# Kernel tuning notes

Measured on AMD Instinct MI355X. Metric: run time of the kernel, lower is better.

Reference implementation:

```python
import jax, jax.numpy as jnp
import numpy as np

# pywt db2 decomposition filters (mode='symmetric', pywt defaults)
DEC_LO = np.array([-0.12940952255092145, 0.22414386804185735,
                   0.836516303737469, 0.48296291314469025], dtype=np.float32)
DEC_HI = np.array([-0.48296291314469025, 0.836516303737469,
                   -0.22414386804185735, -0.12940952255092145], dtype=np.float32)


def _dwt_axis(x, filt, axis):
    """Single-level 1D DWT along `axis`, symmetric padding, matching pywt.

    Equivalent to: symmetric-pad by F-1 each side, full convolution with
    `filt` (true convolution => filter flipped), take indices 1,3,5,...
    Implemented as pad (F-2, F-1) + strided correlation with reversed filter.
    """
    F = filt.shape[0]
    x = jnp.moveaxis(x, axis, -1)
    N = x.shape[-1]
    out_len = (N + F - 1) // 2
    pad = [(0, 0)] * (x.ndim - 1) + [(F - 2, F - 1)]
    xp = jnp.pad(x, pad, mode='symmetric')
    filt_rev = filt[::-1]
    # sum of 4 strided slices (F=4) -- fully vectorized, no big intermediates
    out = filt_rev[0] * xp[..., 0:2 * out_len:2]
    for k in range(1, F):
        out = out + filt_rev[k] * xp[..., k:k + 2 * out_len:2]
    return jnp.moveaxis(out, -1, axis)


def setup_inputs() -> dict:
    key = jax.random.key(0)
    x = jax.random.normal(key, (16, 3, 1024, 1024), dtype=jnp.float32)
    return {"x": x}


def reference(x):
    lo = jnp.asarray(DEC_LO)
    hi = jnp.asarray(DEC_HI)
    # pywt.dwt2 -> cA = 'aa' (approx rows, approx cols),
    #              cH = 'da' (detail along axis -2, approx along axis -1)
    lo_rows = _dwt_axis(x, lo, -2)
    hi_rows = _dwt_axis(x, hi, -2)
    cA = _dwt_axis(lo_rows, lo, -1)
    cH = _dwt_axis(hi_rows, lo, -1)
    return (cA, cH)
```

## Files before the change

### kernel.cpp

```cpp
#include <hip/hip_runtime.h>


#define N 1024
#define NOUT 513
#define TI 8
#define STRIPS ((NOUT + TI - 1) / TI)

__device__ __forceinline__ int refl(int p) {
    int r = p - 2;
    r = (r < 0) ? (-1 - r) : r;
    r = (r > N - 1) ? (2 * N - 1 - r) : r;
    return r;
}

__global__ __launch_bounds__(256, 8) void dwt2_strip(const float* __restrict__ x,
                                                     float* __restrict__ out) {
    const float l0 =  0.48296291314469025f;
    const float l1 =  0.836516303737469f;
    const float l2 =  0.22414386804185735f;
    const float l3 = -0.12940952255092145f;
    const float h0 = -0.12940952255092145f;
    const float h1 = -0.22414386804185735f;
    const float h2 =  0.836516303737469f;
    const float h3 = -0.48296291314469025f;

    __shared__ float sLo[2][N];
    __shared__ float sHi[2][N];

    const int strip = blockIdx.x;
    const int img   = blockIdx.y;
    const int i0 = strip * TI;
    const int t  = threadIdx.x;
    const int c  = 4 * t;

    const float* xim = x + (size_t)img * N * N;
    const size_t plane = (size_t)NOUT * NOUT;
    float* cA = out + (size_t)img * plane;
    float* cH = out + ((size_t)48 + img) * plane;

    const int nrows = (NOUT - i0 < TI) ? (NOUT - i0) : TI;

    float4 r0 = *reinterpret_cast<const float4*>(xim + (size_t)refl(2 * i0)     * N + c);
    float4 r1 = *reinterpret_cast<const float4*>(xim + (size_t)refl(2 * i0 + 1) * N + c);
    float4 n0 = *reinterpret_cast<const float4*>(xim + (size_t)refl(2 * i0 + 2) * N + c);
    float4 n1 = *reinterpret_cast<const float4*>(xim + (size_t)refl(2 * i0 + 3) * N + c);

    for (int ii = 0; ii < nrows; ++ii) {
        const int i = i0 + ii;
        const int buf = ii & 1;

        float4 lo, hi;
        lo.x = l0 * r0.x + l1 * r1.x + l2 * n0.x + l3 * n1.x;
        lo.y = l0 * r0.y + l1 * r1.y + l2 * n0.y + l3 * n1.y;
        lo.z = l0 * r0.z + l1 * r1.z + l2 * n0.z + l3 * n1.z;
        lo.w = l0 * r0.w + l1 * r1.w + l2 * n0.w + l3 * n1.w;
        hi.x = h0 * r0.x + h1 * r1.x + h2 * n0.x + h3 * n1.x;
        hi.y = h0 * r0.y + h1 * r1.y + h2 * n0.y + h3 * n1.y;
        hi.z = h0 * r0.z + h1 * r1.z + h2 * n0.z + h3 * n1.z;
        hi.w = h0 * r0.w + h1 * r1.w + h2 * n0.w + h3 * n1.w;
        *reinterpret_cast<float4*>(&sLo[buf][c]) = lo;
        *reinterpret_cast<float4*>(&sHi[buf][c]) = hi;
        r0 = n0;
        r1 = n1;

        __syncthreads();

        if (ii + 1 < nrows) {
            const int ip = i + 1;
            n0 = *reinterpret_cast<const float4*>(xim + (size_t)refl(2 * ip + 2) * N + c);
            n1 = *reinterpret_cast<const float4*>(xim + (size_t)refl(2 * ip + 3) * N + c);
        }

        const float* __restrict__ Lrow = sLo[buf];
        const float* __restrict__ Hrow = sHi[buf];
        for (int j = t; j < NOUT; j += 256) {
            float a0, a1, a2, a3, b0, b1, b2, b3;
            if (j >= 1 && j <= NOUT - 2) {
                const int cc = 2 * j - 2;
                a0 = Lrow[cc]; a1 = Lrow[cc + 1]; a2 = Lrow[cc + 2]; a3 = Lrow[cc + 3];
                b0 = Hrow[cc]; b1 = Hrow[cc + 1]; b2 = Hrow[cc + 2]; b3 = Hrow[cc + 3];
            } else {
                const int c0 = refl(2 * j), c1 = refl(2 * j + 1);
                const int c2 = refl(2 * j + 2), c3 = refl(2 * j + 3);
                a0 = Lrow[c0]; a1 = Lrow[c1]; a2 = Lrow[c2]; a3 = Lrow[c3];
                b0 = Hrow[c0]; b1 = Hrow[c1]; b2 = Hrow[c2]; b3 = Hrow[c3];
            }
            cA[(size_t)i * NOUT + j] = l0 * a0 + l1 * a1 + l2 * a2 + l3 * a3;
            cH[(size_t)i * NOUT + j] = l0 * b0 + l1 * b1 + l2 * b2 + l3 * b3;
        }
    }
}

extern "C" void kernel_launch(void* const* d_in, const int* in_sizes, int n_in,
                              void* d_out, int out_size, void* d_ws, size_t ws_size,
                              hipStream_t stream) {
    (void)in_sizes; (void)n_in; (void)d_ws; (void)ws_size; (void)out_size;
    const float* x = (const float*)d_in[0];
    float* out = (float*)d_out;
    dim3 grid(STRIPS, 48);
    dim3 block(256);
    dwt2_strip<<<grid, block, 0, stream>>>(x, out);
}
```

Before: 312.7 us.

## Replace shared-memory horizontal pass with wavefront shuffles and register-resident rows

Drops the LDS staging buffers and per-row __syncthreads. Each thread now owns two column pairs and does the horizontal filter with __shfl_up across lanes. Wavefront boundary lanes reload and recompute their neighbours' vertical outputs. This removes block-wide barriers and LDS traffic, at the cost of extra redundant global loads at wave edges, float2 instead of float4 loads, and an odd-column store pattern. It also adds register prefetch of the next rows and lowers the launch-bounds occupancy hint.

```diff
diff --git a/kernel.cpp b/kernel.cpp
--- a/kernel.cpp
+++ b/kernel.cpp
@@ -13,8 +13,16 @@
     return r;
 }
 
-__global__ __launch_bounds__(256, 8) void dwt2_strip(const float* __restrict__ x,
-                                                     float* __restrict__ out) {
+__device__ __forceinline__ float2 vfilt(float f0, float f1, float f2, float f3,
+                                        float2 a, float2 b, float2 c, float2 d) {
+    float2 r;
+    r.x = f0 * a.x + f1 * b.x + f2 * c.x + f3 * d.x;
+    r.y = f0 * a.y + f1 * b.y + f2 * c.y + f3 * d.y;
+    return r;
+}
+
+__global__ __launch_bounds__(256, 4) void dwt2_reg(const float* __restrict__ x,
+                                                   float* __restrict__ out) {
     const float l0 =  0.48296291314469025f;
     const float l1 =  0.836516303737469f;
     const float l2 =  0.22414386804185735f;
@@ -24,71 +32,94 @@
     const float h2 =  0.836516303737469f;
     const float h3 = -0.48296291314469025f;
 
-    __shared__ float sLo[2][N];
-    __shared__ float sHi[2][N];
-
     const int strip = blockIdx.x;
     const int img   = blockIdx.y;
     const int i0 = strip * TI;
     const int t  = threadIdx.x;
-    const int c  = 4 * t;
+    const int lane = t & 63;
 
-    const float* xim = x + (size_t)img * N * N;
+    const float* __restrict__ xim = x + (size_t)img * N * N;
     const size_t plane = (size_t)NOUT * NOUT;
-    float* cA = out + (size_t)img * plane;
-    float* cH = out + ((size_t)48 + img) * plane;
+    float* __restrict__ cA = out + (size_t)img * plane;
+    float* __restrict__ cH = out + ((size_t)48 + img) * plane;
 
-    const int nrows = (NOUT - i0 < TI) ? (NOUT - i0) : TI;
+    int nrows = NOUT - i0; if (nrows > TI) nrows = TI;
 
-    float4 r0 = *reinterpret_cast<const float4*>(xim + (size_t)refl(2 * i0)     * N + c);
-    float4 r1 = *reinterpret_cast<const float4*>(xim + (size_t)refl(2 * i0 + 1) * N + c);
-    float4 n0 = *reinterpret_cast<const float4*>(xim + (size_t)refl(2 * i0 + 2) * N + c);
-    float4 n1 = *reinterpret_cast<const float4*>(xim + (size_t)refl(2 * i0 + 3) * N + c);
+    const int c0 = 2 * t;
+    const int c1 = 2 * t + 512;
+    const bool isb = (lane == 0);
+    const bool b0v = isb && (t != 0);
+
+#define LD2(row, col) (*reinterpret_cast<const float2*>(xim + (size_t)(row) * N + (col)))
+
+    int p = 2 * i0;
+    int ra = refl(p), rb = refl(p + 1), rc = refl(p + 2), rd = refl(p + 3);
+    float2 a00 = LD2(ra, c0), a01 = LD2(rb, c0);
+    float2 b00 = LD2(rc, c0), b01 = LD2(rd, c0);
+    float2 a10 = LD2(ra, c1), a11 = LD2(rb, c1);
+    float2 b10 = LD2(rc, c1), b11 = LD2(rd, c1);
+    float2 am0, am1, bm0, bm1;
+    float2 an0, an1, bn0, bn1;
+    am0 = am1 = bm0 = bm1 = make_float2(0.f, 0.f);
+    an0 = an1 = bn0 = bn1 = make_float2(0.f, 0.f);
+    if (b0v) { am0 = LD2(ra, c0 - 2); am1 = LD2(rb, c0 - 2);
+               bm0 = LD2(rc, c0 - 2); bm1 = LD2(rd, c0 - 2); }
+    if (isb) { an0 = LD2(ra, c1 - 2); an1 = LD2(rb, c1 - 2);
+               bn0 = LD2(rc, c1 - 2); bn1 = LD2(rd, c1 - 2); }
 
     for (int ii = 0; ii < nrows; ++ii) {
         const int i = i0 + ii;
-        const int buf = ii & 1;
 
-        float4 lo, hi;
-        lo.x = l0 * r0.x + l1 * r1.x + l2 * n0.x + l3 * n1.x;
-        lo.y = l0 * r0.y + l1 * r1.y + l2 * n0.y + l3 * n1.y;
-        lo.z = l0 * r0.z + l1 * r1.z + l2 * n0.z + l3 * n1.z;
-        lo.w = l0 * r0.w + l1 * r1.w + l2 * n0.w + l3 * n1.w;
-        hi.x = h0 * r0.x + h1 * r1.x + h2 * n0.x + h3 * n1.x;
-        hi.y = h0 * r0.y + h1 * r1.y + h2 * n0.y + h3 * n1.y;
-        hi.z = h0 * r0.z + h1 * r1.z + h2 * n0.z + h3 * n1.z;
-        hi.w = h0 * r0.w + h1 * r1.w + h2 * n0.w + h3 * n1.w;
-        *reinterpret_cast<float4*>(&sLo[buf][c]) = lo;
-        *reinterpret_cast<float4*>(&sHi[buf][c]) = hi;
-        r0 = n0;
-        r1 = n1;
+        float2 Lo0 = vfilt(l0, l1, l2, l3, a00, a01, b00, b01);
+        float2 Hi0 = vfilt(h0, h1, h2, h3, a00, a01, b00, b01);
+        float2 Lo1 = vfilt(l0, l1, l2, l3, a10, a11, b10, b11);
+        float2 Hi1 = vfilt(h0, h1, h2, h3, a10, a11, b10, b11);
+        float2 LoB0 = vfilt(l0, l1, l2, l3, am0, am1, bm0, bm1);
+        float2 HiB0 = vfilt(h0, h1, h2, h3, am0, am1, bm0, bm1);
+        float2 LoB1 = vfilt(l0, l1, l2, l3, an0, an1, bn0, bn1);
+        float2 HiB1 = vfilt(h0, h1, h2, h3, an0, an1, bn0, bn1);
 
-        __syncthreads();
+        a00 = b00; a01 = b01; a10 = b10; a11 = b11;
+        am0 = bm0; am1 = bm1; an0 = bn0; an1 = bn1;
+        const int pn = 2 * i + 4;
+        const int rn0 = refl(pn), rn1 = refl(pn + 1);
+        b00 = LD2(rn0, c0); b01 = LD2(rn1, c0);
+        b10 = LD2(rn0, c1); b11 = LD2(rn1, c1);
+        if (b0v) { bm0 = LD2(rn0, c0 - 2); bm1 = LD2(rn1, c0 - 2); }
+        if (isb) { bn0 = LD2(rn0, c1 - 2); bn1 = LD2(rn1, c1 - 2); }
 
-        if (ii + 1 < nrows) {
-            const int ip = i + 1;
-            n0 = *reinterpret_cast<const float4*>(xim + (size_t)refl(2 * ip + 2) * N + c);
-            n1 = *reinterpret_cast<const float4*>(xim + (size_t)refl(2 * ip + 3) * N + c);
+        float Lm20 = __shfl_up(Lo0.x, 1);
+        float Lm10 = __shfl_up(Lo0.y, 1);
+        float Hm20 = __shfl_up(Hi0.x, 1);
+        float Hm10 = __shfl_up(Hi0.y, 1);
+        float Lm21 = __shfl_up(Lo1.x, 1);
+        float Lm11 = __shfl_up(Lo1.y, 1);
+        float Hm21 = __shfl_up(Hi1.x, 1);
+        float Hm11 = __shfl_up(Hi1.y, 1);
+        if (isb) {
+            if (t == 0) {
+                Lm20 = Lo0.y; Lm10 = Lo0.x; Hm20 = Hi0.y; Hm10 = Hi0.x;
+            } else {
+                Lm20 = LoB0.x; Lm10 = LoB0.y; Hm20 = HiB0.x; Hm10 = HiB0.y;
+            }
+            Lm21 = LoB1.x; Lm11 = LoB1.y; Hm21 = HiB1.x; Hm11 = HiB1.y;
         }
 
-        const float* __restrict__ Lrow = sLo[buf];
-        const float* __restrict__ Hrow = sHi[buf];
-        for (int j = t; j < NOUT; j += 256) {
-            float a0, a1, a2, a3, b0, b1, b2, b3;
-            if (j >= 1 && j <= NOUT - 2) {
-                const int cc = 2 * j - 2;
-                a0 = Lrow[cc]; a1 = Lrow[cc + 1]; a2 = Lrow[cc + 2]; a3 = Lrow[cc + 3];
-                b0 = Hrow[cc]; b1 = Hrow[cc + 1]; b2 = Hrow[cc + 2]; b3 = Hrow[cc + 3];
-            } else {
-                const int c0 = refl(2 * j), c1 = refl(2 * j + 1);
-                const int c2 = refl(2 * j + 2), c3 = refl(2 * j + 3);
-                a0 = Lrow[c0]; a1 = Lrow[c1]; a2 = Lrow[c2]; a3 = Lrow[c3];
-                b0 = Hrow[c0]; b1 = Hrow[c1]; b2 = Hrow[c2]; b3 = Hrow[c3];
-            }
-            cA[(size_t)i * NOUT + j] = l0 * a0 + l1 * a1 + l2 * a2 + l3 * a3;
-            cH[(size_t)i * NOUT + j] = l0 * b0 + l1 * b1 + l2 * b2 + l3 * b3;
+        const float vA0 = l0 * Lm20 + l1 * Lm10 + l2 * Lo0.x + l3 * Lo0.y;
+        const float vH0 = l0 * Hm20 + l1 * Hm10 + l2 * Hi0.x + l3 * Hi0.y;
+        const float vA1 = l0 * Lm21 + l1 * Lm11 + l2 * Lo1.x + l3 * Lo1.y;
+        const float vH1 = l0 * Hm21 + l1 * Hm11 + l2 * Hi1.x + l3 * Hi1.y;
+        const size_t ro = (size_t)i * NOUT;
+        cA[ro + t] = vA0;
+        cH[ro + t] = vH0;
+        cA[ro + t + 256] = vA1;
+        cH[ro + t + 256] = vH1;
+        if (t == 255) {
+            cA[ro + 512] = (l0 + l3) * Lo1.x + (l1 + l2) * Lo1.y;
+            cH[ro + 512] = (l0 + l3) * Hi1.x + (l1 + l2) * Hi1.y;
         }
     }
+#undef LD2
 }
 
 extern "C" void kernel_launch(void* const* d_in, const int* in_sizes, int n_in,
@@ -99,5 +130,5 @@
     float* out = (float*)d_out;
     dim3 grid(STRIPS, 48);
     dim3 block(256);
-    dwt2_strip<<<grid, block, 0, stream>>>(x, out);
+    dwt2_reg<<<grid, block, 0, stream>>>(x, out);
 }
```

After: 330.8 us. +5.8%, slower.
